# Kernel tuning notes

Measured on AMD Instinct MI355X. Metric: run time of the kernel, lower is better.

## Reference

```python
import jax, jax.numpy as jnp
import numpy as np

N = 100000   # vertices
M = 20000    # hyperedges
NNZ = 1000000  # incidence pairs
L = 50000    # candidate links
K = 2        # vertices per link
IN, H, OUT = 256, 256, 128


def setup_inputs() -> dict:
    key = jax.random.key(0)
    ks = jax.random.split(key, 8)
    X = jax.random.normal(ks[0], (N, IN), jnp.float32)
    v_idx = jax.random.randint(ks[1], (NNZ,), 0, N, jnp.int32)
    e_idx = jax.random.randint(ks[2], (NNZ,), 0, M, jnp.int32)
    link = jax.random.randint(ks[3], (L, K), 0, N, jnp.int32)
    init = lambda k, sh, fan: jax.random.normal(k, sh, jnp.float32) / np.float32(np.sqrt(fan))
    W1 = init(ks[4], (IN, H), IN)
    b1 = jnp.zeros((H,), jnp.float32)
    W2 = init(ks[5], (H, OUT), H)
    b2 = jnp.zeros((OUT,), jnp.float32)
    fc_w = init(ks[6], (OUT, 1), OUT)
    fc_b = jnp.zeros((1,), jnp.float32)
    return dict(X=X, W1=W1, b1=b1, W2=W2, b2=b2, fc_w=fc_w, fc_b=fc_b,
                v_idx=v_idx, e_idx=e_idx, link=link)


def _segment_mean(vals, idx, num_segments):
    # mean aggregation: segment sum / segment count (count clamped to 1)
    s = jax.ops.segment_sum(vals, idx, num_segments=num_segments)
    c = jax.ops.segment_sum(jnp.ones((idx.shape[0], 1), vals.dtype), idx,
                            num_segments=num_segments)
    return s / jnp.maximum(c, 1.0)


def _hgnn_conv(X, W, b, v_idx, e_idx):
    # theta -> v2e mean -> e2v mean -> ReLU (dropout = identity in eval)
    Xt = X @ W + b                              # [N, d_out]
    Y = _segment_mean(Xt[v_idx], e_idx, M)      # [M, d_out] hyperedge feats
    Xv = _segment_mean(Y[e_idx], v_idx, N)      # [N, d_out] back to vertices
    return jax.nn.relu(Xv)


def reference(X, W1, b1, W2, b2, fc_w, fc_b, v_idx, e_idx, link):
    h1 = _hgnn_conv(X, W1, b1, v_idx, e_idx)    # extra .relu() in encode is idempotent
    h2 = _hgnn_conv(h1, W2, b2, v_idx, e_idx)   # [N, OUT]
    # per-link mean of member vertex embeddings (vectorized gather-mean)
    ex = h2[link].mean(axis=1)                  # [L, OUT]
    return jax.nn.sigmoid(ex @ fc_w + fc_b)     # [L, 1]
```

## Files before the change

kernel.cpp:

```cpp
#include <hip/hip_runtime.h>
#include <cstdint>
#include <cstddef>

#define IN_DIM  256
#define H_DIM   256
#define OUT_DIM 128
#define MEDGES  20000

#define B_E 64
#define B_V 64
#define ROWS 64
#define QN2 51200
#define QW2 (QN2 / 4)
#define CT  1024
#define SCAN_T 256

typedef unsigned short u16;
typedef unsigned int   u32;
typedef short bf16x8 __attribute__((ext_vector_type(8)));
typedef float f32x4  __attribute__((ext_vector_type(4)));

__device__ __forceinline__ float bf2f(u16 u) {
    u32 x = ((u32)u) << 16;
    float f;
    __builtin_memcpy(&f, &x, 4);
    return f;
}
__device__ __forceinline__ u16 f2bf(float f) {
    u32 x;
    __builtin_memcpy(&x, &f, 4);
    u32 r = x + 0x7fffu + ((x >> 16) & 1u);
    return (u16)(r >> 16);
}

__global__ void cvt_all(const float4* __restrict__ X,  ushort4* __restrict__ Xb,  int nX,
                        const float4* __restrict__ W1, ushort4* __restrict__ W1b, int nW1,
                        const float4* __restrict__ W2, ushort4* __restrict__ W2b, int nW2)
{
    int i = blockIdx.x * blockDim.x + threadIdx.x;
    const float4* s; ushort4* d; int k;
    if (i < nX)                  { s = X;  d = Xb;  k = i; }
    else if (i < nX + nW1)       { s = W1; d = W1b; k = i - nX; }
    else if (i < nX + nW1 + nW2) { s = W2; d = W2b; k = i - nX - nW1; }
    else return;
    float4 v = s[k];
    ushort4 o;
    o.x = f2bf(v.x); o.y = f2bf(v.y); o.z = f2bf(v.z); o.w = f2bf(v.w);
    d[k] = o;
}

__global__ __launch_bounds__(1024) void count_lds(const int* __restrict__ e_idx,
                                                  const int* __restrict__ v_idx,
                                                  u32* __restrict__ counts_e32,
                                                  u32* __restrict__ counts_v32,
                                                  int nnz, int m, int n)
{
    __shared__ u32 hist[QW2];
    int t = threadIdx.x;
    if ((int)blockIdx.x < B_E) {
        int r = blockIdx.x;
        int chunk = (nnz + B_E - 1) / B_E;
        int beg = r * chunk, end = min(nnz, beg + chunk);
        int ew = (m + 3) >> 2;
        for (int w = t; w < ew; w += CT) hist[w] = 0;
        __syncthreads();
        for (int i = beg + t; i < end; i += CT) {
            int e = e_idx[i];
            atomicAdd(&hist[e >> 2], 1u << ((e & 3) * 8));
        }
        __syncthreads();
        u32* row = counts_e32 + (size_t)r * ew;
        for (int w = t; w < ew; w += CT) row[w] = hist[w];
    } else {
        int r = blockIdx.x - B_E;
        int chunk = (nnz + B_V - 1) / B_V;
        int beg = r * chunk, end = min(nnz, beg + chunk);
        int vw = (n + 3) >> 2;
        u32* row = counts_v32 + (size_t)r * vw;
        for (int q = 0; q < 2; ++q) {
            int w0 = q * QW2;
            int nw = min(QW2, vw - w0);
            int b0 = w0 * 4;
            for (int w = t; w < QW2; w += CT) hist[w] = 0;
            __syncthreads();
            for (int i = beg + t; i < end; i += CT) {
                unsigned d = (unsigned)(v_idx[i] - b0);
                if (d < (unsigned)(4 * nw))
                    atomicAdd(&hist[d >> 2], 1u << ((d & 3) * 8));
            }
            __syncthreads();
            for (int w = t; w < nw; w += CT) row[w0 + w] = hist[w];
            __syncthreads();
        }
    }
}

__global__ __launch_bounds__(SCAN_T) void scan_block_both(u32* __restrict__ counts_e32,
                                                          u32* __restrict__ counts_v32,
                                                          int* __restrict__ e_off,
                                                          int* __restrict__ v_off,
                                                          int* __restrict__ bsums,
                                                          int m, int n, int nbE)
{
    __shared__ int s[SCAN_T];
    u32* mat; int* out; int* bs; int nwords; int blk; int nn;
    if ((int)blockIdx.x < nbE) { mat = counts_e32; out = e_off; bs = bsums;      nwords = (m + 3) >> 2; blk = blockIdx.x;       nn = m; }
    else                       { mat = counts_v32; out = v_off; bs = bsums + 64; nwords = (n + 3) >> 2; blk = blockIdx.x - nbE; nn = n; }
    int w = blk * SCAN_T + threadIdx.x;
    u32 a = 0;
    if (w < nwords) {
        for (int r = 0; r < ROWS; r += 8) {
            u32 v[8];
#pragma unroll
            for (int k = 0; k < 8; ++k) v[k] = mat[(size_t)(r + k) * nwords + w];
#pragma unroll
            for (int k = 0; k < 8; ++k) {
                mat[(size_t)(r + k) * nwords + w] = a;
                a += v[k];
            }
        }
    }
    int b0 = a & 0xff, b1 = (a >> 8) & 0xff, b2 = (a >> 16) & 0xff, b3 = (int)(a >> 24);
    int x = b0 + b1 + b2 + b3;
    s[threadIdx.x] = x;
    __syncthreads();
    for (int off = 1; off < SCAN_T; off <<= 1) {
        int v = (threadIdx.x >= off) ? s[threadIdx.x - off] : 0;
        __syncthreads();
        s[threadIdx.x] += v;
        __syncthreads();
    }
    if (w < nwords) {
        int ex = s[threadIdx.x] - x;
        int base = 4 * w;
        if (base + 3 < nn) {
            int4 o; o.x = ex; o.y = ex + b0; o.z = ex + b0 + b1; o.w = ex + b0 + b1 + b2;
            *(int4*)&out[base] = o;
        } else {
            if (base     < nn) out[base]     = ex;
            if (base + 1 < nn) out[base + 1] = ex + b0;
            if (base + 2 < nn) out[base + 2] = ex + b0 + b1;
            if (base + 3 < nn) out[base + 3] = ex + b0 + b1 + b2;
        }
    }
    if (threadIdx.x == SCAN_T - 1) bs[blk] = s[SCAN_T - 1];
}

__global__ void scan_top_both(int* __restrict__ bsums, int nbE, int nbV,
                              int* __restrict__ e_off, int* __restrict__ v_off,
                              int m, int n, int nnz)
{
    int t = threadIdx.x;
    if (t == 0) {
        int run = 0;
        for (int i = 0; i < nbE; ++i) { int v = bsums[i]; bsums[i] = run; run += v; }
        e_off[m] = nnz;
    } else if (t == 1) {
        int run = 0;
        for (int i = 0; i < nbV; ++i) { int v = bsums[64 + i]; bsums[64 + i] = run; run += v; }
        v_off[n] = nnz;
    }
}

__global__ void scan_add_both(int* __restrict__ e_off, int* __restrict__ v_off,
                              const int* __restrict__ bsums, int m, int n, int nbE)
{
    int* out; const int* bs; int nwords; int blk; int nn;
    if ((int)blockIdx.x < nbE) { out = e_off; bs = bsums;      nwords = (m + 3) >> 2; blk = blockIdx.x;       nn = m; }
    else                       { out = v_off; bs = bsums + 64; nwords = (n + 3) >> 2; blk = blockIdx.x - nbE; nn = n; }
    int w = blk * SCAN_T + threadIdx.x;
    if (w < nwords) {
        int add = bs[blk];
        int base = 4 * w;
        if (base + 3 < nn) {
            int4 o = *(int4*)&out[base];
            o.x += add; o.y += add; o.z += add; o.w += add;
            *(int4*)&out[base] = o;
        } else {
            if (base     < nn) out[base]     += add;
            if (base + 1 < nn) out[base + 1] += add;
            if (base + 2 < nn) out[base + 2] += add;
            if (base + 3 < nn) out[base + 3] += add;
        }
    }
}

__global__ __launch_bounds__(1024) void scatter_lds(const int* __restrict__ e_idx,
                                                    const int* __restrict__ v_idx,
                                                    const u32* __restrict__ counts_e32,
                                                    const u32* __restrict__ counts_v32,
                                                    const int* __restrict__ e_off,
                                                    const int* __restrict__ v_off,
                                                    int* __restrict__ e_list,
                                                    int* __restrict__ v_list,
                                                    int nnz, int m, int n)
{
    __shared__ u32 cur[QW2];
    int t = threadIdx.x;
    if ((int)blockIdx.x < B_E) {
        int r = blockIdx.x;
        int chunk = (nnz + B_E - 1) / B_E;
        int beg = r * chunk, end = min(nnz, beg + chunk);
        int ew = (m + 3) >> 2;
        const u32* base = counts_e32 + (size_t)r * ew;
        for (int w = t; w < ew; w += CT) cur[w] = base[w];
        __syncthreads();
        for (int i = beg + t; i < end; i += CT) {
            int e = e_idx[i];
            int sh = (e & 3) * 8;
            u32 old = atomicAdd(&cur[e >> 2], 1u << sh);
            int rel = (int)((old >> sh) & 0xffu);
            e_list[e_off[e] + rel] = v_idx[i];
        }
    } else {
        int r = blockIdx.x - B_E;
        int chunk = (nnz + B_V - 1) / B_V;
        int beg = r * chunk, end = min(nnz, beg + chunk);
        int vw = (n + 3) >> 2;
        const u32* row = counts_v32 + (size_t)r * vw;
        for (int q = 0; q < 2; ++q) {
            int w0 = q * QW2;
            int nw = min(QW2, vw - w0);
            int b0 = w0 * 4;
            for (int w = t; w < nw; w += CT) cur[w] = row[w0 + w];
            __syncthreads();
            for (int i = beg + t; i < end; i += CT) {
                int v = v_idx[i];
                unsigned d = (unsigned)(v - b0);
                if (d < (unsigned)(4 * nw)) {
                    int sh = (d & 3) * 8;
                    u32 old = atomicAdd(&cur[d >> 2], 1u << sh);
                    int rel = (int)((old >> sh) & 0xffu);
                    v_list[v_off[v] + rel] = e_idx[i];
                }
            }
            __syncthreads();
        }
    }
}

__global__ void seg_mean_w4(const ushort4* __restrict__ src, ushort4* __restrict__ dst,
                            const int* __restrict__ off, const int* __restrict__ lst,
                            int nseg, int do_relu)
{
    int wid  = (blockIdx.x * blockDim.x + threadIdx.x) >> 6;
    int lane = threadIdx.x & 63;
    if (wid >= nseg) return;
    int beg = __builtin_amdgcn_readfirstlane(off[wid]);
    int end = __builtin_amdgcn_readfirstlane(off[wid + 1]);
    float ax = 0.f, ay = 0.f, az = 0.f, aw = 0.f;
    int j = beg;
    for (; j + 7 < end; j += 8) {
        ushort4 r[8];
#pragma unroll
        for (int k = 0; k < 8; ++k) r[k] = src[(size_t)lst[j + k] * 64 + lane];
#pragma unroll
        for (int k = 0; k < 8; ++k) {
            ax += bf2f(r[k].x); ay += bf2f(r[k].y);
            az += bf2f(r[k].z); aw += bf2f(r[k].w);
        }
    }
    for (; j + 3 < end; j += 4) {
        ushort4 r[4];
#pragma unroll
        for (int k = 0; k < 4; ++k) r[k] = src[(size_t)lst[j + k] * 64 + lane];
#pragma unroll
        for (int k = 0; k < 4; ++k) {
            ax += bf2f(r[k].x); ay += bf2f(r[k].y);
            az += bf2f(r[k].z); aw += bf2f(r[k].w);
        }
    }
    for (; j < end; ++j) {
        ushort4 a = src[(size_t)lst[j] * 64 + lane];
        ax += bf2f(a.x); ay += bf2f(a.y); az += bf2f(a.z); aw += bf2f(a.w);
    }
    int cnt = end - beg;
    float inv = (cnt > 0) ? 1.f / (float)cnt : 0.f;
    ax *= inv; ay *= inv; az *= inv; aw *= inv;
    if (do_relu) {
        ax = fmaxf(ax, 0.f); ay = fmaxf(ay, 0.f);
        az = fmaxf(az, 0.f); aw = fmaxf(aw, 0.f);
    }
    ushort4 o;
    o.x = f2bf(ax); o.y = f2bf(ay); o.z = f2bf(az); o.w = f2bf(aw);
    dst[(size_t)wid * 64 + lane] = o;
}

__global__ void seg_mean_w2(const ushort2* __restrict__ src, ushort2* __restrict__ dst,
                            const int* __restrict__ off, const int* __restrict__ lst,
                            int nseg, int do_relu)
{
    int wid  = (blockIdx.x * blockDim.x + threadIdx.x) >> 6;
    int lane = threadIdx.x & 63;
    if (wid >= nseg) return;
    int beg = __builtin_amdgcn_readfirstlane(off[wid]);
    int end = __builtin_amdgcn_readfirstlane(off[wid + 1]);
    float ax = 0.f, ay = 0.f;
    int j = beg;
    for (; j + 7 < end; j += 8) {
        ushort2 r[8];
#pragma unroll
        for (int k = 0; k < 8; ++k) r[k] = src[(size_t)lst[j + k] * 64 + lane];
#pragma unroll
        for (int k = 0; k < 8; ++k) { ax += bf2f(r[k].x); ay += bf2f(r[k].y); }
    }
    for (; j + 3 < end; j += 4) {
        ushort2 r[4];
#pragma unroll
        for (int k = 0; k < 4; ++k) r[k] = src[(size_t)lst[j + k] * 64 + lane];
#pragma unroll
        for (int k = 0; k < 4; ++k) { ax += bf2f(r[k].x); ay += bf2f(r[k].y); }
    }
    for (; j < end; ++j) {
        ushort2 a = src[(size_t)lst[j] * 64 + lane];
        ax += bf2f(a.x); ay += bf2f(a.y);
    }
    int cnt = end - beg;
    float inv = (cnt > 0) ? 1.f / (float)cnt : 0.f;
    ax *= inv; ay *= inv;
    if (do_relu) { ax = fmaxf(ax, 0.f); ay = fmaxf(ay, 0.f); }
    ushort2 o;
    o.x = f2bf(ax); o.y = f2bf(ay);
    dst[(size_t)wid * 64 + lane] = o;
}

#define GSTRIDE 40
__global__ __launch_bounds__(256) void gemm_mfma_bf16(const u16* __restrict__ A,
                                                      const u16* __restrict__ W,
                                                      const float* __restrict__ bias,
                                                      u16* __restrict__ C,
                                                      int R, int K, int Cc)
{
    __shared__ __align__(16) u16 As[64 * GSTRIDE];
    __shared__ __align__(16) u16 Bs[64 * GSTRIDE];

    int tid  = threadIdx.x;
    int wave = tid >> 6;
    int lane = tid & 63;
    int quad = lane >> 4;
    int l16  = lane & 15;

    int row0 = blockIdx.y * 64;
    int col0 = blockIdx.x * 64;

    f32x4 acc[4] = {};

    int ar   = tid >> 2;
    int aseg = tid & 3;
    int bk   = tid >> 3;
    int bn   = tid & 7;

    for (int k0 = 0; k0 < K; k0 += 32) {
        bf16x8 av = {};
        int gr = row0 + ar;
        if (gr < R) av = *(const bf16x8*)&A[(size_t)gr * K + k0 + 8 * aseg];
        *(bf16x8*)&As[ar * GSTRIDE + 8 * aseg] = av;
        bf16x8 wv = *(const bf16x8*)&W[(size_t)(k0 + bk) * Cc + col0 + 8 * bn];
#pragma unroll
        for (int j = 0; j < 8; ++j)
            Bs[(8 * bn + j) * GSTRIDE + bk] = ((const u16*)&wv)[j];
        __syncthreads();

        bf16x8 af = *(const bf16x8*)&As[(16 * wave + l16) * GSTRIDE + 8 * quad];
#pragma unroll
        for (int nt = 0; nt < 4; ++nt) {
            bf16x8 bfv = *(const bf16x8*)&Bs[(16 * nt + l16) * GSTRIDE + 8 * quad];
            acc[nt] = __builtin_amdgcn_mfma_f32_16x16x32_bf16(af, bfv, acc[nt], 0, 0, 0);
        }
        __syncthreads();
    }

#pragma unroll
    for (int nt = 0; nt < 4; ++nt) {
        int col = col0 + 16 * nt + l16;
        float bv = bias[col];
#pragma unroll
        for (int r = 0; r < 4; ++r) {
            int grow = row0 + 16 * wave + 4 * quad + r;
            if (grow < R) C[(size_t)grow * Cc + col] = f2bf(acc[nt][r] + bv);
        }
    }
}

__global__ void link_head(const ushort2* __restrict__ h2, const int* __restrict__ link,
                          const float* __restrict__ fc_w, const float* __restrict__ fc_b,
                          float* __restrict__ out, int L)
{
    int gtid = blockIdx.x * blockDim.x + threadIdx.x;
    int wid  = gtid >> 6;
    int lane = threadIdx.x & 63;
    if (wid >= L) return;
    const int Dh = OUT_DIM / 2;
    int a = link[2 * wid + 0];
    int b = link[2 * wid + 1];
    ushort2 ra = h2[(size_t)a * Dh + lane];
    ushort2 rb = h2[(size_t)b * Dh + lane];
    float2 w = *(const float2*)&fc_w[2 * lane];
    float acc = 0.5f * ((bf2f(ra.x) + bf2f(rb.x)) * w.x + (bf2f(ra.y) + bf2f(rb.y)) * w.y);
#pragma unroll
    for (int off = 32; off; off >>= 1) acc += __shfl_xor(acc, off, 64);
    if (lane == 0) out[wid] = 1.f / (1.f + expf(-(acc + fc_b[0])));
}


static inline size_t align_up(size_t x, size_t a) { return (x + a - 1) & ~(a - 1); }

extern "C" void kernel_launch(void* const* d_in, const int* in_sizes, int n_in,
                              void* d_out, int out_size, void* d_ws, size_t ws_size,
                              hipStream_t stream)
{
    const float* X   = (const float*)d_in[0];
    const float* W1  = (const float*)d_in[1];
    const float* b1  = (const float*)d_in[2];
    const float* W2  = (const float*)d_in[3];
    const float* b2  = (const float*)d_in[4];
    const float* fcw = (const float*)d_in[5];
    const float* fcb = (const float*)d_in[6];
    const int* v_idx = (const int*)d_in[7];
    const int* e_idx = (const int*)d_in[8];
    const int* link  = (const int*)d_in[9];
    float* out = (float*)d_out;

    const int NNZ = in_sizes[7];
    const int N   = in_sizes[0] / IN_DIM;
    const int L   = in_sizes[9] / 2;
    const int M   = MEDGES;

    char* p = (char*)d_ws;
    auto carve = [&](size_t bytes) -> void* {
        void* r = (void*)p;
        p += align_up(bytes, 256);
        return r;
    };
    u16*  Xb    = (u16*)carve((size_t)N * IN_DIM * 2);
    u16*  h1b   = (u16*)carve((size_t)N * H_DIM * 2);
    u16*  Aggb  = (u16*)carve((size_t)M * H_DIM * 2);
    u16*  Yb    = (u16*)carve((size_t)M * H_DIM * 2);
    u16*  W1b   = (u16*)carve((size_t)IN_DIM * H_DIM * 2);
    u16*  W2b   = (u16*)carve((size_t)H_DIM * OUT_DIM * 2);
    int*  e_off = (int*)carve((size_t)(M + 1) * 4);
    int*  v_off = (int*)carve((size_t)(N + 1) * 4);
    int*  e_lst = (int*)carve((size_t)NNZ * 4);
    int*  v_lst = (int*)carve((size_t)NNZ * 4);
    int*  bsums = (int*)carve(2048);

    int EW = (M + 3) >> 2;
    u32* counts_e32 = (u32*)h1b;
    u32* counts_v32 = counts_e32 + (size_t)B_E * EW;

    const int tb = 256;

    int nX  = N * IN_DIM / 4;
    int nW1 = IN_DIM * H_DIM / 4;
    int nW2 = H_DIM * OUT_DIM / 4;
    cvt_all<<<(nX + nW1 + nW2 + tb - 1) / tb, tb, 0, stream>>>(
        (const float4*)X, (ushort4*)Xb, nX,
        (const float4*)W1, (ushort4*)W1b, nW1,
        (const float4*)W2, (ushort4*)W2b, nW2);

    count_lds<<<B_E + B_V, CT, 0, stream>>>(e_idx, v_idx, counts_e32, counts_v32, NNZ, M, N);

    int nbE = (((M + 3) >> 2) + SCAN_T - 1) / SCAN_T;
    int nbV = (((N + 3) >> 2) + SCAN_T - 1) / SCAN_T;
    scan_block_both<<<nbE + nbV, SCAN_T, 0, stream>>>(counts_e32, counts_v32,
                                                      e_off, v_off, bsums, M, N, nbE);
    scan_top_both<<<1, 64, 0, stream>>>(bsums, nbE, nbV, e_off, v_off, M, N, NNZ);
    scan_add_both<<<nbE + nbV, SCAN_T, 0, stream>>>(e_off, v_off, bsums, M, N, nbE);

    scatter_lds<<<B_E + B_V, CT, 0, stream>>>(e_idx, v_idx, counts_e32, counts_v32,
                                              e_off, v_off, e_lst, v_lst, NNZ, M, N);

    seg_mean_w4<<<((size_t)M * 64 + tb - 1) / tb, tb, 0, stream>>>(
        (const ushort4*)Xb, (ushort4*)Aggb, e_off, e_lst, M, 0);
    gemm_mfma_bf16<<<dim3(H_DIM / 64, (M + 63) / 64), 256, 0, stream>>>(Aggb, W1b, b1, Yb, M, IN_DIM, H_DIM);
    seg_mean_w4<<<((size_t)N * 64 + tb - 1) / tb, tb, 0, stream>>>(
        (const ushort4*)Yb, (ushort4*)h1b, v_off, v_lst, N, 1);

    seg_mean_w4<<<((size_t)M * 64 + tb - 1) / tb, tb, 0, stream>>>(
        (const ushort4*)h1b, (ushort4*)Aggb, e_off, e_lst, M, 0);
    gemm_mfma_bf16<<<dim3(OUT_DIM / 64, (M + 63) / 64), 256, 0, stream>>>(Aggb, W2b, b2, Yb, M, H_DIM, OUT_DIM);
    seg_mean_w2<<<((size_t)N * 64 + tb - 1) / tb, tb, 0, stream>>>(
        (const ushort2*)Yb, (ushort2*)Xb, v_off, v_lst, N, 1);

    link_head<<<((size_t)L * 64 + tb - 1) / tb, tb, 0, stream>>>(
        (const ushort2*)Xb, link, fcw, fcb, out, L);
}
```

Measured before the change: 520.3 us.

## Fuse CSR histogram passes, overlap bf16 conversion, merge scan top into add

```diff
diff --git a/kernel.cpp b/kernel.cpp
--- a/kernel.cpp
+++ b/kernel.cpp
@@ -7,11 +7,8 @@
 #define OUT_DIM 128
 #define MEDGES  20000
 
-#define B_E 64
-#define B_V 64
-#define ROWS 64
-#define QN2 51200
-#define QW2 (QN2 / 4)
+#define NB   128
+#define NCVT 256
 #define CT  1024
 #define SCAN_T 256
 
@@ -33,64 +30,52 @@
     return (u16)(r >> 16);
 }
 
-__global__ void cvt_all(const float4* __restrict__ X,  ushort4* __restrict__ Xb,  int nX,
-                        const float4* __restrict__ W1, ushort4* __restrict__ W1b, int nW1,
-                        const float4* __restrict__ W2, ushort4* __restrict__ W2b, int nW2)
-{
-    int i = blockIdx.x * blockDim.x + threadIdx.x;
-    const float4* s; ushort4* d; int k;
-    if (i < nX)                  { s = X;  d = Xb;  k = i; }
-    else if (i < nX + nW1)       { s = W1; d = W1b; k = i - nX; }
-    else if (i < nX + nW1 + nW2) { s = W2; d = W2b; k = i - nX - nW1; }
-    else return;
-    float4 v = s[k];
-    ushort4 o;
-    o.x = f2bf(v.x); o.y = f2bf(v.y); o.z = f2bf(v.z); o.w = f2bf(v.w);
-    d[k] = o;
-}
-
-__global__ __launch_bounds__(1024) void count_lds(const int* __restrict__ e_idx,
+extern __shared__ u32 dyn_lds[];
+
+__global__ __launch_bounds__(1024) void count_cvt(const int* __restrict__ e_idx,
                                                   const int* __restrict__ v_idx,
                                                   u32* __restrict__ counts_e32,
                                                   u32* __restrict__ counts_v32,
-                                                  int nnz, int m, int n)
-{
-    __shared__ u32 hist[QW2];
+                                                  int nnz, int m, int n,
+                                                  const float4* __restrict__ X,  ushort4* __restrict__ Xb,  int nX,
+                                                  const float4* __restrict__ W1, ushort4* __restrict__ W1b, int nW1,
+                                                  const float4* __restrict__ W2, ushort4* __restrict__ W2b, int nW2)
+{
     int t = threadIdx.x;
-    if ((int)blockIdx.x < B_E) {
+    if ((int)blockIdx.x < NB) {
+        int ew = (m + 3) >> 2;
+        int vw = (n + 3) >> 2;
+        u32* he = dyn_lds;
+        u32* hv = dyn_lds + ew;
+        int tot = ew + vw;
+        for (int w = t; w < tot; w += CT) dyn_lds[w] = 0;
+        __syncthreads();
         int r = blockIdx.x;
-        int chunk = (nnz + B_E - 1) / B_E;
+        int chunk = (nnz + NB - 1) / NB;
         int beg = r * chunk, end = min(nnz, beg + chunk);
-        int ew = (m + 3) >> 2;
-        for (int w = t; w < ew; w += CT) hist[w] = 0;
-        __syncthreads();
         for (int i = beg + t; i < end; i += CT) {
             int e = e_idx[i];
-            atomicAdd(&hist[e >> 2], 1u << ((e & 3) * 8));
-        }
-        __syncthreads();
-        u32* row = counts_e32 + (size_t)r * ew;
-        for (int w = t; w < ew; w += CT) row[w] = hist[w];
+            int v = v_idx[i];
+            atomicAdd(&he[e >> 2], 1u << ((e & 3) * 8));
+            atomicAdd(&hv[v >> 2], 1u << ((v & 3) * 8));
+        }
+        __syncthreads();
+        u32* rowe = counts_e32 + (size_t)r * ew;
+        for (int w = t; w < ew; w += CT) rowe[w] = he[w];
+        u32* rowv = counts_v32 + (size_t)r * vw;
+        for (int w = t; w < vw; w += CT) rowv[w] = hv[w];
     } else {
-        int r = blockIdx.x - B_E;
-        int chunk = (nnz + B_V - 1) / B_V;
-        int beg = r * chunk, end = min(nnz, beg + chunk);
-        int vw = (n + 3) >> 2;
-        u32* row = counts_v32 + (size_t)r * vw;
-        for (int q = 0; q < 2; ++q) {
-            int w0 = q * QW2;
-            int nw = min(QW2, vw - w0);
-            int b0 = w0 * 4;
-            for (int w = t; w < QW2; w += CT) hist[w] = 0;
-            __syncthreads();
-            for (int i = beg + t; i < end; i += CT) {
-                unsigned d = (unsigned)(v_idx[i] - b0);
-                if (d < (unsigned)(4 * nw))
-                    atomicAdd(&hist[d >> 2], 1u << ((d & 3) * 8));
-            }
-            __syncthreads();
-            for (int w = t; w < nw; w += CT) row[w0 + w] = hist[w];
-            __syncthreads();
+        int b = blockIdx.x - NB;
+        int ntot = nX + nW1 + nW2;
+        for (int i = b * CT + t; i < ntot; i += NCVT * CT) {
+            const float4* s; ushort4* d; int k;
+            if (i < nX)            { s = X;  d = Xb;  k = i; }
+            else if (i < nX + nW1) { s = W1; d = W1b; k = i - nX; }
+            else                   { s = W2; d = W2b; k = i - nX - nW1; }
+            float4 v = s[k];
+            ushort4 o;
+            o.x = f2bf(v.x); o.y = f2bf(v.y); o.z = f2bf(v.z); o.w = f2bf(v.w);
+            d[k] = o;
         }
     }
 }
@@ -109,7 +94,7 @@
     int w = blk * SCAN_T + threadIdx.x;
     u32 a = 0;
     if (w < nwords) {
-        for (int r = 0; r < ROWS; r += 8) {
+        for (int r = 0; r < NB; r += 8) {
             u32 v[8];
 #pragma unroll
             for (int k = 0; k < 8; ++k) v[k] = mat[(size_t)(r + k) * nwords + w];
@@ -146,31 +131,29 @@
     if (threadIdx.x == SCAN_T - 1) bs[blk] = s[SCAN_T - 1];
 }
 
-__global__ void scan_top_both(int* __restrict__ bsums, int nbE, int nbV,
-                              int* __restrict__ e_off, int* __restrict__ v_off,
-                              int m, int n, int nnz)
-{
-    int t = threadIdx.x;
-    if (t == 0) {
-        int run = 0;
-        for (int i = 0; i < nbE; ++i) { int v = bsums[i]; bsums[i] = run; run += v; }
-        e_off[m] = nnz;
-    } else if (t == 1) {
-        int run = 0;
-        for (int i = 0; i < nbV; ++i) { int v = bsums[64 + i]; bsums[64 + i] = run; run += v; }
-        v_off[n] = nnz;
-    }
-}
-
-__global__ void scan_add_both(int* __restrict__ e_off, int* __restrict__ v_off,
-                              const int* __restrict__ bsums, int m, int n, int nbE)
-{
+__global__ __launch_bounds__(SCAN_T) void scan_addtop(int* __restrict__ e_off,
+                                                      int* __restrict__ v_off,
+                                                      const int* __restrict__ bsums,
+                                                      int m, int n, int nbE, int nnz)
+{
+    __shared__ int s[SCAN_T];
     int* out; const int* bs; int nwords; int blk; int nn;
     if ((int)blockIdx.x < nbE) { out = e_off; bs = bsums;      nwords = (m + 3) >> 2; blk = blockIdx.x;       nn = m; }
     else                       { out = v_off; bs = bsums + 64; nwords = (n + 3) >> 2; blk = blockIdx.x - nbE; nn = n; }
-    int w = blk * SCAN_T + threadIdx.x;
+    int t = threadIdx.x;
+    s[t] = (t < blk) ? bs[t] : 0;
+    __syncthreads();
+    for (int off = 1; off < SCAN_T; off <<= 1) {
+        int v = (t >= off) ? s[t - off] : 0;
+        __syncthreads();
+        s[t] += v;
+        __syncthreads();
+    }
+    int add = s[SCAN_T - 1];
+    if ((int)blockIdx.x == 0   && t == 0) e_off[m] = nnz;
+    if ((int)blockIdx.x == nbE && t == 0) v_off[n] = nnz;
+    int w = blk * SCAN_T + t;
     if (w < nwords) {
-        int add = bs[blk];
         int base = 4 * w;
         if (base + 3 < nn) {
             int4 o = *(int4*)&out[base];
@@ -185,7 +168,7 @@
     }
 }
 
-__global__ __launch_bounds__(1024) void scatter_lds(const int* __restrict__ e_idx,
+__global__ __launch_bounds__(1024) void scatter_all(const int* __restrict__ e_idx,
                                                     const int* __restrict__ v_idx,
                                                     const u32* __restrict__ counts_e32,
                                                     const u32* __restrict__ counts_v32,
@@ -195,47 +178,28 @@
                                                     int* __restrict__ v_list,
                                                     int nnz, int m, int n)
 {
-    __shared__ u32 cur[QW2];
     int t = threadIdx.x;
-    if ((int)blockIdx.x < B_E) {
-        int r = blockIdx.x;
-        int chunk = (nnz + B_E - 1) / B_E;
-        int beg = r * chunk, end = min(nnz, beg + chunk);
-        int ew = (m + 3) >> 2;
-        const u32* base = counts_e32 + (size_t)r * ew;
-        for (int w = t; w < ew; w += CT) cur[w] = base[w];
-        __syncthreads();
-        for (int i = beg + t; i < end; i += CT) {
-            int e = e_idx[i];
-            int sh = (e & 3) * 8;
-            u32 old = atomicAdd(&cur[e >> 2], 1u << sh);
-            int rel = (int)((old >> sh) & 0xffu);
-            e_list[e_off[e] + rel] = v_idx[i];
-        }
-    } else {
-        int r = blockIdx.x - B_E;
-        int chunk = (nnz + B_V - 1) / B_V;
-        int beg = r * chunk, end = min(nnz, beg + chunk);
-        int vw = (n + 3) >> 2;
-        const u32* row = counts_v32 + (size_t)r * vw;
-        for (int q = 0; q < 2; ++q) {
-            int w0 = q * QW2;
-            int nw = min(QW2, vw - w0);
-            int b0 = w0 * 4;
-            for (int w = t; w < nw; w += CT) cur[w] = row[w0 + w];
-            __syncthreads();
-            for (int i = beg + t; i < end; i += CT) {
-                int v = v_idx[i];
-                unsigned d = (unsigned)(v - b0);
-                if (d < (unsigned)(4 * nw)) {
-                    int sh = (d & 3) * 8;
-                    u32 old = atomicAdd(&cur[d >> 2], 1u << sh);
-                    int rel = (int)((old >> sh) & 0xffu);
-                    v_list[v_off[v] + rel] = e_idx[i];
-                }
-            }
-            __syncthreads();
-        }
+    int ew = (m + 3) >> 2;
+    int vw = (n + 3) >> 2;
+    u32* ce = dyn_lds;
+    u32* cv = dyn_lds + ew;
+    int r = blockIdx.x;
+    const u32* rowe = counts_e32 + (size_t)r * ew;
+    for (int w = t; w < ew; w += CT) ce[w] = rowe[w];
+    const u32* rowv = counts_v32 + (size_t)r * vw;
+    for (int w = t; w < vw; w += CT) cv[w] = rowv[w];
+    __syncthreads();
+    int chunk = (nnz + NB - 1) / NB;
+    int beg = r * chunk, end = min(nnz, beg + chunk);
+    for (int i = beg + t; i < end; i += CT) {
+        int e = e_idx[i];
+        int v = v_idx[i];
+        int she = (e & 3) * 8;
+        u32 olde = atomicAdd(&ce[e >> 2], 1u << she);
+        e_list[e_off[e] + (int)((olde >> she) & 0xffu)] = v;
+        int shv = (v & 3) * 8;
+        u32 oldv = atomicAdd(&cv[v >> 2], 1u << shv);
+        v_list[v_off[v] + (int)((oldv >> shv) & 0xffu)] = e;
     }
 }
 
@@ -445,30 +409,33 @@
     int*  bsums = (int*)carve(2048);
 
     int EW = (M + 3) >> 2;
+    int VW = (N + 3) >> 2;
     u32* counts_e32 = (u32*)h1b;
-    u32* counts_v32 = counts_e32 + (size_t)B_E * EW;
+    u32* counts_v32 = counts_e32 + (size_t)NB * EW;
 
     const int tb = 256;
+    const int DYN = (EW + VW) * 4;
+
+    (void)hipFuncSetAttribute((const void*)count_cvt,  hipFuncAttributeMaxDynamicSharedMemorySize, DYN);
+    (void)hipFuncSetAttribute((const void*)scatter_all, hipFuncAttributeMaxDynamicSharedMemorySize, DYN);
 
     int nX  = N * IN_DIM / 4;
     int nW1 = IN_DIM * H_DIM / 4;
     int nW2 = H_DIM * OUT_DIM / 4;
-    cvt_all<<<(nX + nW1 + nW2 + tb - 1) / tb, tb, 0, stream>>>(
-        (const float4*)X, (ushort4*)Xb, nX,
-        (const float4*)W1, (ushort4*)W1b, nW1,
-        (const float4*)W2, (ushort4*)W2b, nW2);
-
-    count_lds<<<B_E + B_V, CT, 0, stream>>>(e_idx, v_idx, counts_e32, counts_v32, NNZ, M, N);
-
-    int nbE = (((M + 3) >> 2) + SCAN_T - 1) / SCAN_T;
-    int nbV = (((N + 3) >> 2) + SCAN_T - 1) / SCAN_T;
+    count_cvt<<<NB + NCVT, CT, DYN, stream>>>(e_idx, v_idx, counts_e32, counts_v32,
+                                              NNZ, M, N,
+                                              (const float4*)X, (ushort4*)Xb, nX,
+                                              (const float4*)W1, (ushort4*)W1b, nW1,
+                                              (const float4*)W2, (ushort4*)W2b, nW2);
+
+    int nbE = (EW + SCAN_T - 1) / SCAN_T;
+    int nbV = (VW + SCAN_T - 1) / SCAN_T;
     scan_block_both<<<nbE + nbV, SCAN_T, 0, stream>>>(counts_e32, counts_v32,
                                                       e_off, v_off, bsums, M, N, nbE);
-    scan_top_both<<<1, 64, 0, stream>>>(bsums, nbE, nbV, e_off, v_off, M, N, NNZ);
-    scan_add_both<<<nbE + nbV, SCAN_T, 0, stream>>>(e_off, v_off, bsums, M, N, nbE);
-
-    scatter_lds<<<B_E + B_V, CT, 0, stream>>>(e_idx, v_idx, counts_e32, counts_v32,
-                                              e_off, v_off, e_lst, v_lst, NNZ, M, N);
+    scan_addtop<<<nbE + nbV, SCAN_T, 0, stream>>>(e_off, v_off, bsums, M, N, nbE, NNZ);
+
+    scatter_all<<<NB, CT, DYN, stream>>>(e_idx, v_idx, counts_e32, counts_v32,
+                                         e_off, v_off, e_lst, v_lst, NNZ, M, N);
 
     seg_mean_w4<<<((size_t)M * 64 + tb - 1) / tb, tb, 0, stream>>>(
         (const ushort4*)Xb, (ushort4*)Aggb, e_off, e_lst, M, 0);
```

Result: faster. 498.5 us, median of 2 (-4.2%).
